# Kernel tuning notes

Hardware: AMD Instinct MI355X
Metric: run time of the kernel (lower is better)

## Reference

```python
import jax, jax.numpy as jnp
import numpy as np

B, S, D = 4, 4096, 1024
H, HID, ATT = 16, 64, 64


def setup_inputs() -> dict:
    key = jax.random.key(0)
    ks = jax.random.split(key, 7)
    sc = 0.02
    return {
        "x": jax.random.normal(ks[0], (B, S, D), dtype=jnp.float32),
        "Wq": jax.random.normal(ks[1], (D, H * HID), dtype=jnp.float32) * sc,
        "bq": jnp.zeros((H * HID,), dtype=jnp.float32),
        "Wk": jax.random.normal(ks[2], (D, H * HID), dtype=jnp.float32) * sc,
        "bk": jnp.zeros((H * HID,), dtype=jnp.float32),
        "Wv": jax.random.normal(ks[3], (D, H * ATT), dtype=jnp.float32) * sc,
        "bv": jnp.zeros((H * ATT,), dtype=jnp.float32),
    }


def reference(x, Wq, bq, Wk, bk, Wv, bv):
    b, s, _ = x.shape
    q = (x @ Wq + bq).reshape(b, s, H, HID)
    k = (x @ Wk + bk).reshape(b, s, H, HID)
    v = (x @ Wv + bv).reshape(b, s, H, ATT)
    # attention across the head axis: [B,S,H,H] scores per token
    scores = jnp.einsum("bsid,bsjd->bsij", q, k) / np.sqrt(HID).astype(np.float32)
    probs = jax.nn.softmax(scores, axis=-1)
    ctx = jnp.einsum("bsij,bsja->bsia", probs, v)
    return ctx.reshape(b, s, H * ATT)
```

## Files before the change

### kernel.cpp

```cpp
#include <hip/hip_runtime.h>


#define AS1 __attribute__((address_space(1)))
#define AS3 __attribute__((address_space(3)))

typedef __bf16 bf16x8 __attribute__((ext_vector_type(8)));
typedef float f32x4 __attribute__((ext_vector_type(4)));
typedef float f32x16 __attribute__((ext_vector_type(16)));
typedef unsigned short u16x8 __attribute__((ext_vector_type(8)));

static constexpr int MTOK = 16384;
static constexpr int N3   = 3072;
static constexpr int KD   = 1024;
static constexpr int NT   = KD / 64;

__device__ __forceinline__ unsigned short f2bf(float f) {
  unsigned u = __float_as_uint(f);
  unsigned r = u + 0x7FFFu + ((u >> 16) & 1u);
  return (unsigned short)(r >> 16);
}
__device__ __forceinline__ float bf2f(unsigned short s) {
  return __uint_as_float(((unsigned)s) << 16);
}

__device__ __forceinline__ void gload_lds16(const void* g, void* lds_uniform) {
  __builtin_amdgcn_global_load_lds((const AS1 void*)g, (AS3 void*)lds_uniform, 16, 0, 0);
}

__global__ __launch_bounds__(256) void cvt_x_kernel(const float* __restrict__ x,
                                                    unsigned short* __restrict__ xb) {
  int i = blockIdx.x * 256 + threadIdx.x;
  const float4* p = (const float4*)x;
  float4 a = p[2 * i], b = p[2 * i + 1];
  u16x8 o;
  o[0] = f2bf(a.x); o[1] = f2bf(a.y); o[2] = f2bf(a.z); o[3] = f2bf(a.w);
  o[4] = f2bf(b.x); o[5] = f2bf(b.y); o[6] = f2bf(b.z); o[7] = f2bf(b.w);
  *((u16x8*)xb + i) = o;
}

__global__ __launch_bounds__(256) void prep_w_kernel(const float* __restrict__ Wq,
                                                     const float* __restrict__ Wk,
                                                     const float* __restrict__ Wv,
                                                     const float* __restrict__ bq,
                                                     const float* __restrict__ bk,
                                                     const float* __restrict__ bv,
                                                     unsigned short* __restrict__ WT,
                                                     float* __restrict__ bcat) {
  __shared__ float tile[32][33];
  int kt = blockIdx.x * 32;
  int nt = blockIdx.y * 32;
  const float* W; const float* bias; int nb;
  if (nt < 1024)      { W = Wq; bias = bq; nb = nt; }
  else if (nt < 2048) { W = Wk; bias = bk; nb = nt - 1024; }
  else                { W = Wv; bias = bv; nb = nt - 2048; }
  int tx = threadIdx.x & 31, ty = threadIdx.x >> 5;
#pragma unroll
  for (int it = 0; it < 4; ++it) {
    int kk = it * 8 + ty;
    tile[kk][tx] = W[(size_t)(kt + kk) * 1024 + nb + tx];
  }
  __syncthreads();
#pragma unroll
  for (int it = 0; it < 4; ++it) {
    int nn = it * 8 + ty;
    WT[(size_t)(nt + nn) * 1024 + kt + tx] = f2bf(tile[tx][nn]);
  }
  if (blockIdx.x == 0 && threadIdx.x < 32)
    bcat[nt + threadIdx.x] = bias[nb + threadIdx.x];
}

__global__ __launch_bounds__(512, 2) void gemm_qkv_kernel(const unsigned short* __restrict__ A,
                                                          const unsigned short* __restrict__ Bt,
                                                          const float* __restrict__ bias,
                                                          unsigned short* __restrict__ C) {
  __shared__ __align__(16) unsigned short lds[65536];
  const int tid  = threadIdx.x;
  const int lane = tid & 63;
  const int wave = tid >> 6;
  const int wm = wave >> 2, wn = wave & 3;
  const int m0 = blockIdx.x * 256;
  const int n0 = blockIdx.y * 256;

  const int sp_ = tid >> 3;
  const int srow = sp_ * 4 + (tid & 3);
  const int sh   = ((tid >> 2) & 1) ^ (sp_ & 1);
  const size_t asrc = (size_t)(m0 + srow) * KD + sh * 8;
  const size_t bsrc = (size_t)(n0 + srow) * KD + sh * 8;

  int aoff[4], boff[2];
#pragma unroll
  for (int m = 0; m < 4; ++m) {
    int row = wm * 128 + m * 32 + (lane & 31);
    int p = row >> 2;
    aoff[m] = (p * 128 + (((lane >> 5) ^ (p & 1)) * 4 + (row & 3)) * 16) >> 1;
  }
#pragma unroll
  for (int n = 0; n < 2; ++n) {
    int row = wn * 64 + n * 32 + (lane & 31);
    int p = row >> 2;
    boff[n] = 4096 + ((p * 128 + (((lane >> 5) ^ (p & 1)) * 4 + (row & 3)) * 16) >> 1);
  }

  f32x16 acc[4][2] = {};

#define STAGE(T, P)                                                            \
  do {                                                                         \
    unsigned short* dst = lds + ((T) & 1) * 32768 + (P) * 8192 + tid * 8;      \
    const int kk = (T) * 64 + (P) * 16;                                        \
    gload_lds16(A  + asrc + kk, dst);                                          \
    gload_lds16(Bt + bsrc + kk, dst + 4096);                                   \
  } while (0)

#define PHASE(T, P, DOSTAGE, ST, SSL)                                          \
  do {                                                                         \
    const unsigned short* bufp = lds + ((T) & 1) * 32768 + (P) * 8192;         \
    bf16x8 af[4], bfr[2];                                                      \
    _Pragma("unroll") for (int m = 0; m < 4; ++m)                              \
      af[m] = *(const bf16x8*)(bufp + aoff[m]);                                \
    _Pragma("unroll") for (int n = 0; n < 2; ++n)                              \
      bfr[n] = *(const bf16x8*)(bufp + boff[n]);                               \
    asm volatile("s_waitcnt lgkmcnt(0)" ::: "memory");                         \
    __builtin_amdgcn_sched_barrier(0);                                         \
    __builtin_amdgcn_s_barrier();                                              \
    if (DOSTAGE) { STAGE(ST, SSL); }                                           \
    __builtin_amdgcn_sched_barrier(0);                                         \
    __builtin_amdgcn_s_setprio(1);                                             \
    _Pragma("unroll") for (int m = 0; m < 4; ++m)                              \
      _Pragma("unroll") for (int n = 0; n < 2; ++n)                            \
        acc[m][n] = __builtin_amdgcn_mfma_f32_32x32x16_bf16(af[m], bfr[n],     \
                                                            acc[m][n], 0, 0, 0);\
    __builtin_amdgcn_s_setprio(0);                                             \
  } while (0)

  STAGE(0, 0); STAGE(0, 1); STAGE(0, 2); STAGE(0, 3);
  STAGE(1, 0); STAGE(1, 1); STAGE(1, 2);

#pragma unroll 1
  for (int t = 0; t < NT - 2; ++t) {
    asm volatile("s_waitcnt vmcnt(6)" ::: "memory");
    __builtin_amdgcn_s_barrier();
    PHASE(t, 0, true, t + 1, 3);
    PHASE(t, 1, true, t + 2, 0);
    PHASE(t, 2, true, t + 2, 1);
    PHASE(t, 3, true, t + 2, 2);
  }
  asm volatile("s_waitcnt vmcnt(6)" ::: "memory");
  __builtin_amdgcn_s_barrier();
  PHASE(NT - 2, 0, true, NT - 1, 3);
  PHASE(NT - 2, 1, false, 0, 0);
  PHASE(NT - 2, 2, false, 0, 0);
  PHASE(NT - 2, 3, false, 0, 0);
  asm volatile("s_waitcnt vmcnt(0)" ::: "memory");
  __builtin_amdgcn_s_barrier();
  PHASE(NT - 1, 0, false, 0, 0);
  PHASE(NT - 1, 1, false, 0, 0);
  PHASE(NT - 1, 2, false, 0, 0);
  PHASE(NT - 1, 3, false, 0, 0);
#undef STAGE
#undef PHASE

#pragma unroll
  for (int n = 0; n < 2; ++n) {
    int col = n0 + wn * 64 + n * 32 + (lane & 31);
    float bvv = bias[col];
#pragma unroll
    for (int m = 0; m < 4; ++m) {
      int rowb = m0 + wm * 128 + m * 32 + 4 * (lane >> 5);
#pragma unroll
      for (int r = 0; r < 16; ++r) {
        int row = rowb + (r & 3) + 8 * (r >> 2);
        C[(size_t)row * N3 + col] = f2bf(acc[m][n][r] + bvv);
      }
    }
  }
}

__global__ __launch_bounds__(256) void attn_kernel(const unsigned short* __restrict__ qkv,
                                                   float* __restrict__ out) {
  __shared__ float p_lds[4][16][17];
  const int tid = threadIdx.x;
  const int lane = tid & 63;
  const int w = tid >> 6;
  const size_t token = (size_t)blockIdx.x * 4 + w;
  const unsigned short* rowp = qkv + token * N3;
  const int head = lane & 15;
  const int chunk = lane >> 4;

  const int o = head * 64 + chunk * 8;
  bf16x8 q0 = *(const bf16x8*)(rowp + o);
  bf16x8 q1 = *(const bf16x8*)(rowp + o + 32);
  bf16x8 k0 = *(const bf16x8*)(rowp + 1024 + o);
  bf16x8 k1 = *(const bf16x8*)(rowp + 1024 + o + 32);
  f32x4 c = {0.f, 0.f, 0.f, 0.f};
  c = __builtin_amdgcn_mfma_f32_16x16x32_bf16(q0, k0, c, 0, 0, 0);
  c = __builtin_amdgcn_mfma_f32_16x16x32_bf16(q1, k1, c, 0, 0, 0);

#pragma unroll
  for (int r = 0; r < 4; ++r) {
    float s = c[r] * 0.125f;
    float m = s;
#pragma unroll
    for (int off = 1; off < 16; off <<= 1) m = fmaxf(m, __shfl_xor(m, off, 64));
    float e = __expf(s - m);
    float sum = e;
#pragma unroll
    for (int off = 1; off < 16; off <<= 1) sum += __shfl_xor(sum, off, 64);
    p_lds[w][chunk * 4 + r][head] = e / sum;
  }
  __syncthreads();

  const int i = lane >> 2;
  const int ab = lane & 3;
  const unsigned short* vbase = rowp + 2048 + ab * 16;
  float accv[16];
#pragma unroll
  for (int cc = 0; cc < 16; ++cc) accv[cc] = 0.f;
#pragma unroll
  for (int j = 0; j < 16; ++j) {
    float pij = p_lds[w][i][j];
    u16x8 v0 = *(const u16x8*)(vbase + j * 64);
    u16x8 v1 = *(const u16x8*)(vbase + j * 64 + 8);
#pragma unroll
    for (int cc = 0; cc < 8; ++cc) accv[cc] += pij * bf2f(v0[cc]);
#pragma unroll
    for (int cc = 0; cc < 8; ++cc) accv[8 + cc] += pij * bf2f(v1[cc]);
  }
  float* op = out + token * 1024 + i * 64 + ab * 16;
#pragma unroll
  for (int cc = 0; cc < 16; cc += 4) {
    f32x4 v = {accv[cc], accv[cc + 1], accv[cc + 2], accv[cc + 3]};
    *(f32x4*)(op + cc) = v;
  }
}

extern "C" void kernel_launch(void* const* d_in, const int* in_sizes, int n_in,
                              void* d_out, int out_size, void* d_ws, size_t ws_size,
                              hipStream_t stream) {
  const float* x  = (const float*)d_in[0];
  const float* Wq = (const float*)d_in[1];
  const float* bq = (const float*)d_in[2];
  const float* Wk = (const float*)d_in[3];
  const float* bk = (const float*)d_in[4];
  const float* Wv = (const float*)d_in[5];
  const float* bv = (const float*)d_in[6];
  float* out = (float*)d_out;

  char* ws = (char*)d_ws;
  unsigned short* xb   = (unsigned short*)ws;
  unsigned short* WT   = (unsigned short*)(ws + 33554432);
  float*          bcat = (float*)(ws + 39845888);
  unsigned short* qkv  = (unsigned short*)(ws + 39858176);

  cvt_x_kernel<<<dim3((MTOK * KD / 8) / 256), 256, 0, stream>>>(x, xb);
  prep_w_kernel<<<dim3(32, 96), 256, 0, stream>>>(Wq, Wk, Wv, bq, bk, bv, WT, bcat);
  gemm_qkv_kernel<<<dim3(MTOK / 256, N3 / 256), 512, 0, stream>>>(xb, WT, bcat, qkv);
  attn_kernel<<<dim3(MTOK / 4), 256, 0, stream>>>(qkv, out);
}
```

Measured before the change: 193.1 us.

## Restructure QKV GEMM LDS pipeline into two half-K stages with new swizzle

Reorganizes the QKV projection GEMM's LDS staging from four 16-wide K slices per 64-K tile into two 32-wide slices. Each slice has its own row-based XOR swizzle, and each thread issues four global-to-LDS loads per stage. Each phase now issues its stage loads right after its LDS fragment reads and runs 16 MFMAs instead of 8. This halves the number of barriers per K tile and gives more compute to hide global load latency. In exchange it needs more fragment registers, and the different swizzle and vmcnt accounting may change LDS bank conflicts and correctness margins.

Result: faster. 171.9 us (-11.0%).

```diff
diff --git a/kernel.cpp b/kernel.cpp
--- a/kernel.cpp
+++ b/kernel.cpp
@@ -81,83 +81,88 @@
   const int m0 = blockIdx.x * 256;
   const int n0 = blockIdx.y * 256;
 
-  const int sp_ = tid >> 3;
-  const int srow = sp_ * 4 + (tid & 3);
-  const int sh   = ((tid >> 2) & 1) ^ (sp_ & 1);
-  const size_t asrc = (size_t)(m0 + srow) * KD + sh * 8;
-  const size_t bsrc = (size_t)(n0 + srow) * KD + sh * 8;
-
-  int aoff[4], boff[2];
+  const int srow = tid >> 2;
+  const int sc   = ((tid & 3) ^ ((srow >> 1) & 3)) * 8;
+  const size_t asrc0 = (size_t)(m0 + srow) * KD + sc;
+  const size_t asrc1 = (size_t)(m0 + 128 + srow) * KD + sc;
+  const size_t bsrc0 = (size_t)(n0 + srow) * KD + sc;
+  const size_t bsrc1 = (size_t)(n0 + 128 + srow) * KD + sc;
+
+  int aoff[4][2], boff[2][2];
 #pragma unroll
   for (int m = 0; m < 4; ++m) {
     int row = wm * 128 + m * 32 + (lane & 31);
-    int p = row >> 2;
-    aoff[m] = (p * 128 + (((lane >> 5) ^ (p & 1)) * 4 + (row & 3)) * 16) >> 1;
+#pragma unroll
+    for (int ks = 0; ks < 2; ++ks) {
+      int pc = (ks * 2 + (lane >> 5)) ^ ((row >> 1) & 3);
+      aoff[m][ks] = row * 32 + pc * 8;
+    }
   }
 #pragma unroll
   for (int n = 0; n < 2; ++n) {
     int row = wn * 64 + n * 32 + (lane & 31);
-    int p = row >> 2;
-    boff[n] = 4096 + ((p * 128 + (((lane >> 5) ^ (p & 1)) * 4 + (row & 3)) * 16) >> 1);
+#pragma unroll
+    for (int ks = 0; ks < 2; ++ks) {
+      int pc = (ks * 2 + (lane >> 5)) ^ ((row >> 1) & 3);
+      boff[n][ks] = 8192 + row * 32 + pc * 8;
+    }
   }
 
   f32x16 acc[4][2] = {};
 
-#define STAGE(T, P)                                                            \
+#define STAGE(T, S)                                                            \
   do {                                                                         \
-    unsigned short* dst = lds + ((T) & 1) * 32768 + (P) * 8192 + tid * 8;      \
-    const int kk = (T) * 64 + (P) * 16;                                        \
-    gload_lds16(A  + asrc + kk, dst);                                          \
-    gload_lds16(Bt + bsrc + kk, dst + 4096);                                   \
+    unsigned short* dst = lds + ((T) & 1) * 32768 + (S) * 16384 + tid * 8;     \
+    const int kk = (T) * 64 + (S) * 32;                                        \
+    gload_lds16(A  + asrc0 + kk, dst);                                         \
+    gload_lds16(A  + asrc1 + kk, dst + 4096);                                  \
+    gload_lds16(Bt + bsrc0 + kk, dst + 8192);                                  \
+    gload_lds16(Bt + bsrc1 + kk, dst + 12288);                                 \
   } while (0)
 
-#define PHASE(T, P, DOSTAGE, ST, SSL)                                          \
+#define PHASE(T, S, DOSTAGE, ST, SS)                                           \
   do {                                                                         \
-    const unsigned short* bufp = lds + ((T) & 1) * 32768 + (P) * 8192;         \
-    bf16x8 af[4], bfr[2];                                                      \
+    const unsigned short* bufp = lds + ((T) & 1) * 32768 + (S) * 16384;        \
+    bf16x8 af[4][2], bfr[2][2];                                                \
     _Pragma("unroll") for (int m = 0; m < 4; ++m)                              \
-      af[m] = *(const bf16x8*)(bufp + aoff[m]);                                \
+      _Pragma("unroll") for (int ks = 0; ks < 2; ++ks)                         \
+        af[m][ks] = *(const bf16x8*)(bufp + aoff[m][ks]);                      \
     _Pragma("unroll") for (int n = 0; n < 2; ++n)                              \
-      bfr[n] = *(const bf16x8*)(bufp + boff[n]);                               \
+      _Pragma("unroll") for (int ks = 0; ks < 2; ++ks)                         \
+        bfr[n][ks] = *(const bf16x8*)(bufp + boff[n][ks]);                     \
+    if (DOSTAGE) { STAGE(ST, SS); }                                            \
     asm volatile("s_waitcnt lgkmcnt(0)" ::: "memory");                         \
     __builtin_amdgcn_sched_barrier(0);                                         \
-    __builtin_amdgcn_s_barrier();                                              \
-    if (DOSTAGE) { STAGE(ST, SSL); }                                           \
-    __builtin_amdgcn_sched_barrier(0);                                         \
     __builtin_amdgcn_s_setprio(1);                                             \
-    _Pragma("unroll") for (int m = 0; m < 4; ++m)                              \
-      _Pragma("unroll") for (int n = 0; n < 2; ++n)                            \
-        acc[m][n] = __builtin_amdgcn_mfma_f32_32x32x16_bf16(af[m], bfr[n],     \
-                                                            acc[m][n], 0, 0, 0);\
+    _Pragma("unroll") for (int ks = 0; ks < 2; ++ks)                           \
+      _Pragma("unroll") for (int m = 0; m < 4; ++m)                            \
+        _Pragma("unroll") for (int n = 0; n < 2; ++n)                          \
+          acc[m][n] = __builtin_amdgcn_mfma_f32_32x32x16_bf16(af[m][ks],       \
+                          bfr[n][ks], acc[m][n], 0, 0, 0);                     \
     __builtin_amdgcn_s_setprio(0);                                             \
   } while (0)
 
-  STAGE(0, 0); STAGE(0, 1); STAGE(0, 2); STAGE(0, 3);
-  STAGE(1, 0); STAGE(1, 1); STAGE(1, 2);
+#define SYNC(VM)                                                               \
+  do {                                                                         \
+    asm volatile("s_waitcnt vmcnt(" #VM ")" ::: "memory");                     \
+    __builtin_amdgcn_s_barrier();                                              \
+    __builtin_amdgcn_sched_barrier(0);                                         \
+  } while (0)
+
+  STAGE(0, 0); STAGE(0, 1); STAGE(1, 0);
 
 #pragma unroll 1
   for (int t = 0; t < NT - 2; ++t) {
-    asm volatile("s_waitcnt vmcnt(6)" ::: "memory");
-    __builtin_amdgcn_s_barrier();
-    PHASE(t, 0, true, t + 1, 3);
-    PHASE(t, 1, true, t + 2, 0);
-    PHASE(t, 2, true, t + 2, 1);
-    PHASE(t, 3, true, t + 2, 2);
-  }
-  asm volatile("s_waitcnt vmcnt(6)" ::: "memory");
-  __builtin_amdgcn_s_barrier();
-  PHASE(NT - 2, 0, true, NT - 1, 3);
-  PHASE(NT - 2, 1, false, 0, 0);
-  PHASE(NT - 2, 2, false, 0, 0);
-  PHASE(NT - 2, 3, false, 0, 0);
-  asm volatile("s_waitcnt vmcnt(0)" ::: "memory");
-  __builtin_amdgcn_s_barrier();
-  PHASE(NT - 1, 0, false, 0, 0);
-  PHASE(NT - 1, 1, false, 0, 0);
-  PHASE(NT - 1, 2, false, 0, 0);
-  PHASE(NT - 1, 3, false, 0, 0);
+    SYNC(8); PHASE(t, 0, true, t + 1, 1);
+    SYNC(8); PHASE(t, 1, true, t + 2, 0);
+  }
+  SYNC(8); PHASE(NT - 2, 0, true, NT - 1, 1);
+  SYNC(8); PHASE(NT - 2, 1, false, 0, 0);
+  SYNC(4); PHASE(NT - 1, 0, false, 0, 0);
+  SYNC(0); PHASE(NT - 1, 1, false, 0, 0);
 #undef STAGE
 #undef PHASE
+#undef SYNC
 
 #pragma unroll
   for (int n = 0; n < 2; ++n) {
```
